# Optimization experiments

Hardware: AMD Instinct MI355X
Metric: run time of the kernel (lower is better)

The kernel has to match this reference:

```python
import jax, jax.numpy as jnp
import numpy as np
from jax import lax

B, T, N, C = 32, 32, 64, 64          # batch, window, num_series, inter_dim
GRU_H, QK, HOR = 64, 32, 12          # gru_dim, qk_dim, prediction_horizon
KS = (3, 5, 7)                       # temporal kernel per block (3 + 2*i)


def setup_inputs() -> dict:
    key = jax.random.key(0)
    ks = jax.random.split(key, 32)
    rn = lambda k, shape, s=0.05: jax.random.normal(k, shape, jnp.float32) * s
    inp = {"x": jax.random.normal(ks[0], (B, T, N), jnp.float32)}
    # x_to_inter_dim: Conv1d(1, C, kernel_size=1) == scalar * w + b
    inp["w_x2i"] = rn(ks[1], (C,)); inp["b_x2i"] = rn(ks[2], (C,))
    # latentCorrelation GRU (input_size=1, hidden=GRU_H), gate order r,z,n
    inp["gru_wih"] = rn(ks[3], (3 * GRU_H, 1)); inp["gru_whh"] = rn(ks[4], (3 * GRU_H, GRU_H))
    inp["gru_bih"] = rn(ks[5], (3 * GRU_H,)); inp["gru_bhh"] = rn(ks[6], (3 * GRU_H,))
    inp["wq_w"] = rn(ks[7], (QK, GRU_H)); inp["wq_b"] = rn(ks[8], (QK,))
    inp["wk_w"] = rn(ks[9], (QK, GRU_H)); inp["wk_b"] = rn(ks[10], (QK,))
    # per block: T independent GCNConvs (theta + bias), one temporal Conv1d
    for i, k_ in enumerate(KS):
        inp[f"gcn_w{i}"] = rn(ks[11 + 4 * i], (T, C, C))
        inp[f"gcn_b{i}"] = rn(ks[12 + 4 * i], (T, C))
        inp[f"conv_w{i}"] = rn(ks[13 + 4 * i], (C, C, k_))
        inp[f"conv_b{i}"] = rn(ks[14 + 4 * i], (C,))
    inp["lout_w"] = rn(ks[25], (N * HOR, T * N * C), 0.01)
    inp["lout_b"] = rn(ks[26], (N * HOR,))
    return inp


def _forward(x, w_x2i, b_x2i, gru_wih, gru_whh, gru_bih, gru_bhh,
             wq_w, wq_b, wk_w, wk_b,
             gcn_w0, gcn_b0, conv_w0, conv_b0,
             gcn_w1, gcn_b1, conv_w1, conv_b1,
             gcn_w2, gcn_b2, conv_w2, conv_b2,
             lout_w, lout_b):
    xs = jnp.transpose(x, (1, 0, 2))  # (T, B, N) time-major

    # --- latentCorrelation: one GRU run over all B*N series at once ---
    def gru_step(h, xt):  # h: (B,N,GRU_H), xt: (B,N)
        gi = xt[..., None] * gru_wih[:, 0] + gru_bih           # (B,N,3H)
        gh = h @ gru_whh.T + gru_bhh                           # (B,N,3H)
        r = jax.nn.sigmoid(gi[..., :GRU_H] + gh[..., :GRU_H])
        z = jax.nn.sigmoid(gi[..., GRU_H:2 * GRU_H] + gh[..., GRU_H:2 * GRU_H])
        n = jnp.tanh(gi[..., 2 * GRU_H:] + r * gh[..., 2 * GRU_H:])
        return (1.0 - z) * n + z * h, None

    h0 = jnp.zeros((B, N, GRU_H), x.dtype)
    hT, _ = lax.scan(gru_step, h0, xs)                         # (B,N,GRU_H)
    Q = hT @ wq_w.T + wq_b                                     # (B,N,QK)
    K = hT @ wk_w.T + wk_b
    Wadj = jax.nn.softmax(jnp.einsum('bnq,bmq->bnm', Q, K) / jnp.sqrt(jnp.float32(QK)), axis=2)

    # GCN symmetric norm on the dense complete graph; edge (src=i, tgt=j) has
    # weight Wadj[b,i,j]; degree is per-target (column) sum.
    deg = Wadj.sum(axis=1)                                     # (B,N)
    dinv = jnp.where(deg > 0, 1.0 / jnp.sqrt(deg), 0.0)
    What = dinv[:, :, None] * Wadj * dinv[:, None, :]          # (B,N,N)

    # x_to_inter_dim (1x1 conv) applied per timestep
    feats = xs[..., None] * w_x2i + b_x2i                      # (T,B,N,C)

    for gw, gb, cw, cb, k_ in ((gcn_w0, gcn_b0, conv_w0, conv_b0, 3),
                               (gcn_w1, gcn_b1, conv_w1, conv_b1, 5),
                               (gcn_w2, gcn_b2, conv_w2, conv_b2, 7)):
        xw = jnp.einsum('tbnc,tcd->tbnd', feats, gw)           # per-timestep theta
        agg = jnp.einsum('bij,tbid->tbjd', What, xw) + gb[:, None, None, :]
        seq = jnp.transpose(agg, (1, 2, 3, 0)).reshape(B * N, C, T)
        p = k_ // 2
        conv = lax.conv_general_dilated(seq, cw, (1,), [(p, p)],
                                        dimension_numbers=('NCH', 'OIH', 'NCH'))
        conv = conv + cb[None, :, None]
        conv = jnp.where(conv >= 0, conv, 0.01 * conv)         # LeakyReLU (dropout p=0)
        feats = jnp.transpose(conv.reshape(B, N, C, T), (3, 0, 1, 2))

    # stack(x_list, dim=2).view(B*N, C*T).view(B, -1) -> (B, N*C*T) feature order (n,c,t)
    flat = jnp.transpose(feats, (1, 2, 3, 0)).reshape(B, N * C * T)
    out = flat @ lout_w.T + lout_b                             # (B, N*HOR)
    return out.reshape(B, HOR, N)


def reference(x, w_x2i, b_x2i, gru_wih, gru_whh, gru_bih, gru_bhh,
              wq_w, wq_b, wk_w, wk_b,
              gcn_w0, gcn_b0, conv_w0, conv_b0,
              gcn_w1, gcn_b1, conv_w1, conv_b1,
              gcn_w2, gcn_b2, conv_w2, conv_b2,
              lout_w, lout_b):
    return _forward(x, w_x2i, b_x2i, gru_wih, gru_whh, gru_bih, gru_bhh,
                    wq_w, wq_b, wk_w, wk_b,
                    gcn_w0, gcn_b0, conv_w0, conv_b0,
                    gcn_w1, gcn_b1, conv_w1, conv_b1,
                    gcn_w2, gcn_b2, conv_w2, conv_b2,
                    lout_w, lout_b)
```

## Files before the change

kernel.cpp:

```cpp
#include <hip/hip_runtime.h>
#include <hip/hip_bf16.h>

#define BB 32
#define TT 32
#define NN 64
#define CC 64
#define HH 64
#define QKD 32
#define HOR 12
#define OUTD (NN*HOR)
#define KFLAT (NN*CC*TT)

typedef __attribute__((ext_vector_type(4))) float f32x4;
typedef __attribute__((ext_vector_type(8))) short s16x8;
typedef unsigned short ush;

static __device__ __forceinline__ ush f2bf(float f) {
    unsigned u = __float_as_uint(f);
    unsigned r = (u + 0x7FFFu + ((u >> 16) & 1u)) >> 16;
    return (ush)r;
}
static __device__ __forceinline__ float bf2f(ush h) {
    return __uint_as_float(((unsigned)h) << 16);
}
static __device__ __forceinline__ void split8(const float* f, uint4& hi, uint4& lo) {
    unsigned hh[8], ll[8];
    #pragma unroll
    for (int i = 0; i < 8; ++i) {
        ush h = f2bf(f[i]);
        float hf = bf2f(h);
        hh[i] = h;
        ll[i] = f2bf(f[i] - hf);
    }
    hi = make_uint4(hh[0] | (hh[1] << 16), hh[2] | (hh[3] << 16),
                    hh[4] | (hh[5] << 16), hh[6] | (hh[7] << 16));
    lo = make_uint4(ll[0] | (ll[1] << 16), ll[2] | (ll[3] << 16),
                    ll[4] | (ll[5] << 16), ll[6] | (ll[7] << 16));
}
static __device__ __forceinline__ void gl2lds16(const void* gsrc, void* ldst) {
    __builtin_amdgcn_global_load_lds(
        (const __attribute__((address_space(1))) unsigned int*)gsrc,
        (__attribute__((address_space(3))) unsigned int*)ldst, 16, 0, 0);
}

__global__ __launch_bounds__(256) void prep_gru_kernel(
    const float* __restrict__ x, const float* __restrict__ wih,
    const float* __restrict__ whh, const float* __restrict__ bih,
    const float* __restrict__ bhh, float* __restrict__ hT,
    const float* __restrict__ gw0, const float* __restrict__ wx, const float* __restrict__ bx,
    float* __restrict__ u, float* __restrict__ v,
    const float* __restrict__ gw1, ush* __restrict__ g1h, ush* __restrict__ g1l,
    const float* __restrict__ gw2, ush* __restrict__ g2h, ush* __restrict__ g2l,
    const float* __restrict__ cw1, ush* __restrict__ c1h, ush* __restrict__ c1l,
    const float* __restrict__ cw2, ush* __restrict__ c2h, ush* __restrict__ c2l,
    const float* __restrict__ cw3, ush* __restrict__ c3h, ush* __restrict__ c3l,
    const float* __restrict__ lb, float* __restrict__ out)
{
    __shared__ __align__(16) char smem[17408];
    int bid = blockIdx.x, tid = threadIdx.x;

    if (bid < 32) {
        float (*pu)[64] = (float(*)[64])smem;
        float (*pv)[64] = (float(*)[64])(smem + 1024);
        int t = bid, d = tid & 63, cq = tid >> 6;
        float su = 0.f, sv = 0.f;
        for (int c = cq*16; c < cq*16 + 16; ++c) {
            float gv = gw0[t*4096 + c*64 + d];
            su += wx[c]*gv; sv += bx[c]*gv;
        }
        pu[cq][d] = su; pv[cq][d] = sv;
        __syncthreads();
        if (tid < 64) {
            u[t*64 + tid] = pu[0][tid]+pu[1][tid]+pu[2][tid]+pu[3][tid];
            v[t*64 + tid] = pv[0][tid]+pv[1][tid]+pv[2][tid]+pv[3][tid];
        }
    } else if (bid < 96) {
        const float* gw = (bid < 64) ? gw1 : gw2;
        ush* hi = (bid < 64) ? g1h : g2h;
        ush* lo = (bid < 64) ? g1l : g2l;
        int t = (bid < 64) ? bid - 32 : bid - 64;
        for (int idx = tid; idx < 4096; idx += 256) {
            int d = idx >> 6, c = idx & 63;
            float val = gw[t*4096 + c*64 + d];
            ush h = f2bf(val);
            hi[t*4096 + idx] = h;
            lo[t*4096 + idx] = f2bf(val - bf2f(h));
        }
    } else if (bid < 288) {
        const float* cw; ush *hi, *lo; int KW, co;
        if (bid < 160)      { cw = cw1; hi = c1h; lo = c1l; KW = 3; co = bid - 96; }
        else if (bid < 224) { cw = cw2; hi = c2h; lo = c2l; KW = 5; co = bid - 160; }
        else                { cw = cw3; hi = c3h; lo = c3l; KW = 7; co = bid - 224; }
        int K = KW*64;
        for (int idx = tid; idx < K; idx += 256) {
            int ka = idx >> 6, ci = idx & 63;
            float val = cw[(size_t)(co*64 + ci)*KW + ka];
            ush h = f2bf(val);
            hi[(size_t)co*K + idx] = h;
            lo[(size_t)co*K + idx] = f2bf(val - bf2f(h));
        }
    } else if (bid < 384) {
        int idx = (bid - 288)*256 + tid;
        out[idx] = lb[idx % OUTD];
    }
    __syncthreads();

    {
        float (*hbuf)[64] = (float(*)[64])smem;
        float4* part = (float4*)(smem + 1024);
        int w = tid >> 6, j = tid & 63;
        float Wreg[3][16];
        #pragma unroll
        for (int g = 0; g < 3; ++g)
            #pragma unroll
            for (int q = 0; q < 4; ++q) {
                float4 wv = *(const float4*)&whh[(g*64 + j)*64 + w*16 + q*4];
                Wreg[g][q*4+0] = wv.x; Wreg[g][q*4+1] = wv.y;
                Wreg[g][q*4+2] = wv.z; Wreg[g][q*4+3] = wv.w;
            }
        hbuf[w][j] = 0.0f;
        int gs0 = bid * 4;
        int b = gs0 >> 6, n0 = gs0 & 63;
        float wih_r = wih[j], wih_z = wih[64+j], wih_n = wih[128+j];
        float bi_r = bih[j], bi_z = bih[64+j], bi_n = bih[128+j];
        float bh_r = bhh[j], bh_z = bhh[64+j], bh_n = bhh[128+j];
        __syncthreads();
        float hreg = 0.0f;
        for (int t = 0; t < TT; ++t) {
            float p[3][4];
            #pragma unroll
            for (int g = 0; g < 3; ++g)
                #pragma unroll
                for (int s = 0; s < 4; ++s) p[g][s] = 0.f;
            #pragma unroll
            for (int s = 0; s < 4; ++s) {
                #pragma unroll
                for (int q = 0; q < 4; ++q) {
                    const float4 hv = *(const float4*)&hbuf[s][w*16 + q*4];
                    #pragma unroll
                    for (int g = 0; g < 3; ++g) {
                        p[g][s] += hv.x*Wreg[g][q*4]   + hv.y*Wreg[g][q*4+1]
                                 + hv.z*Wreg[g][q*4+2] + hv.w*Wreg[g][q*4+3];
                    }
                }
            }
            #pragma unroll
            for (int s = 0; s < 4; ++s)
                part[(w*4 + s)*64 + j] = make_float4(p[0][s], p[1][s], p[2][s], 0.f);
            __syncthreads();
            float4 q0 = part[(0*4 + w)*64 + j];
            float4 q1 = part[(1*4 + w)*64 + j];
            float4 q2 = part[(2*4 + w)*64 + j];
            float4 q3 = part[(3*4 + w)*64 + j];
            float gr = bh_r + q0.x + q1.x + q2.x + q3.x;
            float gz = bh_z + q0.y + q1.y + q2.y + q3.y;
            float gn = bh_n + q0.z + q1.z + q2.z + q3.z;
            float xt = x[(b*TT + t)*NN + n0 + w];
            float r = 1.f/(1.f+__expf(-(xt*wih_r + bi_r + gr)));
            float z = 1.f/(1.f+__expf(-(xt*wih_z + bi_z + gz)));
            float nn_ = tanhf(xt*wih_n + bi_n + r*gn);
            float hnew = (1.f - z)*nn_ + z*hreg;
            hreg = hnew;
            hbuf[w][j] = hnew;
            __syncthreads();
        }
        hT[(gs0 + w)*64 + j] = hreg;
    }
}

__global__ __launch_bounds__(256) void attn_kernel(
    const float* __restrict__ hT, const float* __restrict__ wq_w,
    const float* __restrict__ wq_b, const float* __restrict__ wk_w,
    const float* __restrict__ wk_b,
    ush* __restrict__ whT_hi, ush* __restrict__ whT_lo)
{
    __shared__ float hs[64][64];
    __shared__ float Qs[64][33], Ks[64][33];
    __shared__ float S[64][65];
    __shared__ float pd[4][64];
    __shared__ float dinv[64];
    int b = blockIdx.x, tid = threadIdx.x;
    for (int idx = tid; idx < 64*64; idx += 256) hs[idx>>6][idx&63] = hT[b*4096 + idx];
    __syncthreads();
    for (int idx = tid; idx < 64*32; idx += 256) {
        int n_ = idx >> 5, q = idx & 31;
        float accq = wq_b[q], acck = wk_b[q];
        #pragma unroll 8
        for (int h_ = 0; h_ < 64; ++h_) {
            float hv = hs[n_][h_];
            accq += hv * wq_w[q*64 + h_];
            acck += hv * wk_w[q*64 + h_];
        }
        Qs[n_][q] = accq; Ks[n_][q] = acck;
    }
    __syncthreads();
    const float scale = 0.17677669529663687f;
    for (int idx = tid; idx < 64*64; idx += 256) {
        int n_ = idx >> 6, m = idx & 63;
        float acc = 0.f;
        #pragma unroll 8
        for (int q = 0; q < 32; ++q) acc += Qs[n_][q]*Ks[m][q];
        S[n_][m] = acc * scale;
    }
    __syncthreads();
    {
        int r = tid >> 2, q = tid & 3;
        float mx = -1e30f;
        #pragma unroll
        for (int m = 0; m < 16; ++m) mx = fmaxf(mx, S[r][q*16+m]);
        mx = fmaxf(mx, __shfl_xor(mx, 1));
        mx = fmaxf(mx, __shfl_xor(mx, 2));
        float sum = 0.f;
        float e[16];
        #pragma unroll
        for (int m = 0; m < 16; ++m) { e[m] = __expf(S[r][q*16+m]-mx); sum += e[m]; }
        sum += __shfl_xor(sum, 1);
        sum += __shfl_xor(sum, 2);
        float inv = 1.f/sum;
        #pragma unroll
        for (int m = 0; m < 16; ++m) S[r][q*16+m] = e[m]*inv;
    }
    __syncthreads();
    {
        int c = tid & 63, rq = tid >> 6;
        float d = 0.f;
        #pragma unroll
        for (int i = 0; i < 16; ++i) d += S[rq*16 + i][c];
        pd[rq][c] = d;
    }
    __syncthreads();
    if (tid < 64) {
        float d = pd[0][tid]+pd[1][tid]+pd[2][tid]+pd[3][tid];
        dinv[tid] = (d > 0.f) ? 1.0f/sqrtf(d) : 0.f;
    }
    __syncthreads();
    for (int idx = tid; idx < 64*64; idx += 256) {
        int jj = idx >> 6, ii = idx & 63;
        float val = dinv[ii]*S[ii][jj]*dinv[jj];
        ush h = f2bf(val);
        whT_hi[b*4096 + idx] = h;
        whT_lo[b*4096 + idx] = f2bf(val - bf2f(h));
    }
}

template<bool FIRST>
__global__ __launch_bounds__(256) void gcn_mfma(
    const float* __restrict__ fin,
    const ush* __restrict__ gwT_hi, const ush* __restrict__ gwT_lo,
    const float* __restrict__ u, const float* __restrict__ v,
    const ush* __restrict__ whT_hi, const ush* __restrict__ whT_lo,
    const float* __restrict__ gb, float* __restrict__ o)
{
    __shared__ __align__(16) ush ft_hi[64][64], ft_lo[64][64];
    __shared__ __align__(16) ush xsT_hi[64][64], xsT_lo[64][64];
    __shared__ float x_l[64];
    int tb = blockIdx.x, t = tb >> 5, b = tb & 31;
    int tid = threadIdx.x;
    int w = tid >> 6, l = tid & 63, lm = l & 15, ld = l >> 4;

    if (FIRST) {
        if (tid < 64) x_l[tid] = fin[(b*TT + t)*NN + tid];
        __syncthreads();
        int d = tid >> 2, nq = tid & 3;
        float ud = u[t*64 + d], vd = v[t*64 + d];
        float vals[16];
        #pragma unroll
        for (int i = 0; i < 16; ++i) vals[i] = x_l[nq*16 + i]*ud + vd;
        #pragma unroll
        for (int h = 0; h < 2; ++h) {
            uint4 hi, lo; split8(&vals[h*8], hi, lo);
            int un = (nq*2 + h) ^ (d & 7);
            *(uint4*)&xsT_hi[d][un*8] = hi;
            *(uint4*)&xsT_lo[d][un*8] = lo;
        }
        __syncthreads();
    } else {
        {
            int row = tid >> 2, c0 = (tid & 3) * 16;
            const float* src = fin + (size_t)tb*4096 + row*64 + c0;
            float f8a[8], f8b[8];
            *(float4*)f8a = *(const float4*)src;       *(float4*)(f8a+4) = *(const float4*)(src+4);
            *(float4*)f8b = *(const float4*)(src+8);   *(float4*)(f8b+4) = *(const float4*)(src+12);
            uint4 hi, lo;
            split8(f8a, hi, lo);
            int u0 = ((c0>>3)) ^ (row & 7);
            *(uint4*)&ft_hi[row][u0*8] = hi; *(uint4*)&ft_lo[row][u0*8] = lo;
            split8(f8b, hi, lo);
            int u1 = ((c0>>3)+1) ^ (row & 7);
            *(uint4*)&ft_hi[row][u1*8] = hi; *(uint4*)&ft_lo[row][u1*8] = lo;
        }
        __syncthreads();
        f32x4 acc[4];
        #pragma unroll
        for (int ct = 0; ct < 4; ++ct) acc[ct] = (f32x4){0.f,0.f,0.f,0.f};
        #pragma unroll
        for (int kc = 0; kc < 2; ++kc) {
            int nrow = w*16 + lm;
            int ux = (kc*4 + ld) ^ (nrow & 7);
            s16x8 xh = *(const s16x8*)&ft_hi[nrow][ux*8];
            s16x8 xl = *(const s16x8*)&ft_lo[nrow][ux*8];
            #pragma unroll
            for (int ct = 0; ct < 4; ++ct) {
                int drow = ct*16 + lm;
                s16x8 yh = *(const s16x8*)&gwT_hi[t*4096 + drow*64 + kc*32 + ld*8];
                s16x8 yl = *(const s16x8*)&gwT_lo[t*4096 + drow*64 + kc*32 + ld*8];
                acc[ct] = __builtin_amdgcn_mfma_f32_16x16x32_bf16(xh, yh, acc[ct], 0, 0, 0);
                acc[ct] = __builtin_amdgcn_mfma_f32_16x16x32_bf16(xh, yl, acc[ct], 0, 0, 0);
                acc[ct] = __builtin_amdgcn_mfma_f32_16x16x32_bf16(xl, yh, acc[ct], 0, 0, 0);
            }
        }
        #pragma unroll
        for (int ct = 0; ct < 4; ++ct) {
            int d = ct*16 + lm;
            int n0 = w*16 + ld*4;
            ush hh[4], llo[4];
            #pragma unroll
            for (int r = 0; r < 4; ++r) {
                float val = acc[ct][r];
                ush h = f2bf(val);
                hh[r] = h; llo[r] = f2bf(val - bf2f(h));
            }
            int un = (n0 >> 3) ^ (d & 7);
            int base = d*64 + un*8 + (n0 & 7);
            *(uint2*)&xsT_hi[0][0 + base] = make_uint2(hh[0]|(hh[1]<<16), hh[2]|(hh[3]<<16));
            *(uint2*)&xsT_lo[0][0 + base] = make_uint2(llo[0]|(llo[1]<<16), llo[2]|(llo[3]<<16));
        }
        __syncthreads();
    }

    f32x4 acc2[4];
    #pragma unroll
    for (int ct = 0; ct < 4; ++ct) acc2[ct] = (f32x4){0.f,0.f,0.f,0.f};
    #pragma unroll
    for (int kc = 0; kc < 2; ++kc) {
        int jrow = w*16 + lm;
        s16x8 wh = *(const s16x8*)&whT_hi[b*4096 + jrow*64 + kc*32 + ld*8];
        s16x8 wl = *(const s16x8*)&whT_lo[b*4096 + jrow*64 + kc*32 + ld*8];
        #pragma unroll
        for (int ct = 0; ct < 4; ++ct) {
            int drow = ct*16 + lm;
            int uy = (kc*4 + ld) ^ (drow & 7);
            s16x8 yh = *(const s16x8*)&xsT_hi[drow][uy*8];
            s16x8 yl = *(const s16x8*)&xsT_lo[drow][uy*8];
            acc2[ct] = __builtin_amdgcn_mfma_f32_16x16x32_bf16(wh, yh, acc2[ct], 0, 0, 0);
            acc2[ct] = __builtin_amdgcn_mfma_f32_16x16x32_bf16(wh, yl, acc2[ct], 0, 0, 0);
            acc2[ct] = __builtin_amdgcn_mfma_f32_16x16x32_bf16(wl, yh, acc2[ct], 0, 0, 0);
        }
    }
    float* oo = o + (size_t)tb*4096;
    #pragma unroll
    for (int ct = 0; ct < 4; ++ct) {
        int d = ct*16 + lm;
        float bias = gb[t*64 + d];
        #pragma unroll
        for (int r = 0; r < 4; ++r) {
            int jj = w*16 + ld*4 + r;
            oo[jj*64 + d] = acc2[ct][r] + bias;
        }
    }
}

template<int KW, bool LAST>
__global__ __launch_bounds__(256) void conv_mfma(float* __restrict__ g,
    const ush* __restrict__ wch, const ush* __restrict__ wcl,
    const float* __restrict__ cb, ush* __restrict__ fo)
{
    constexpr int P = KW/2, K = KW*64, K32 = KW*2;
    __shared__ __align__(16) ush sh[32][64], sl[32][64];
    int bn = blockIdx.x, tid = threadIdx.x;
    {
        int t = tid >> 3, c0 = (tid & 7) * 8;
        const float* src = &g[((size_t)t*2048 + bn)*64 + c0];
        float f8[8];
        *(float4*)f8 = *(const float4*)src;
        *(float4*)(f8+4) = *(const float4*)(src+4);
        uint4 hi, lo; split8(f8, hi, lo);
        int uu = (tid & 7) ^ (t & 7);
        *(uint4*)&sh[t][uu*8] = hi;
        *(uint4*)&sl[t][uu*8] = lo;
    }
    __syncthreads();
    int w = tid >> 6, l = tid & 63, lm = l & 15, ld = l >> 4;
    int co = w*16 + lm;
    f32x4 acc0 = {0.f,0.f,0.f,0.f}, acc1 = {0.f,0.f,0.f,0.f};
    const s16x8 zf = {0,0,0,0,0,0,0,0};
    for (int kc = 0; kc < K32; ++kc) {
        int ka = kc >> 1;
        int ci = (kc & 1)*32 + ld*8;
        s16x8 yh = *(const s16x8*)&wch[(size_t)co*K + kc*32 + ld*8];
        s16x8 yl = *(const s16x8*)&wcl[(size_t)co*K + kc*32 + ld*8];
        #pragma unroll
        for (int Mt = 0; Mt < 2; ++Mt) {
            int ts = Mt*16 + lm + ka - P;
            bool ok = ((unsigned)ts) < 32u;
            int tc = ok ? ts : 0;
            int ua = (ci >> 3) ^ (tc & 7);
            s16x8 xh = *(const s16x8*)&sh[tc][ua*8];
            s16x8 xl = *(const s16x8*)&sl[tc][ua*8];
            if (!ok) { xh = zf; xl = zf; }
            f32x4& a = Mt ? acc1 : acc0;
            a = __builtin_amdgcn_mfma_f32_16x16x32_bf16(xh, yh, a, 0, 0, 0);
            a = __builtin_amdgcn_mfma_f32_16x16x32_bf16(xh, yl, a, 0, 0, 0);
            a = __builtin_amdgcn_mfma_f32_16x16x32_bf16(xl, yh, a, 0, 0, 0);
        }
    }
    float bias = cb[co];
    if (LAST) {
        int b = bn >> 6, n = bn & 63;
        ush* ob = fo + (size_t)b*KFLAT + n*2048 + co*32;
        #pragma unroll
        for (int Mt = 0; Mt < 2; ++Mt) {
            const f32x4& a = Mt ? acc1 : acc0;
            ush hv[4];
            #pragma unroll
            for (int r = 0; r < 4; ++r) {
                float val = a[r] + bias;
                val = (val >= 0.f) ? val : 0.01f*val;
                hv[r] = f2bf(val);
            }
            *(uint2*)&ob[Mt*16 + ld*4] = make_uint2(hv[0]|(hv[1]<<16), hv[2]|(hv[3]<<16));
        }
    } else {
        #pragma unroll
        for (int Mt = 0; Mt < 2; ++Mt) {
            const f32x4& a = Mt ? acc1 : acc0;
            #pragma unroll
            for (int r = 0; r < 4; ++r) {
                int t = Mt*16 + ld*4 + r;
                float val = a[r] + bias;
                val = (val >= 0.f) ? val : 0.01f*val;
                g[((size_t)t*2048 + bn)*64 + co] = val;
            }
        }
    }
}

__global__ __launch_bounds__(256) void gemm_mfma(const ush* __restrict__ flat,
                                                 const float* __restrict__ W,
                                                 float* __restrict__ out)
{
    __shared__ __align__(16) float Wl[2][64][64];
    __shared__ __align__(16) ush Al[2][32][64];
    const int tid = threadIdx.x;
    const int w = tid >> 6, l = tid & 63;
    const int og = blockIdx.x >> 6;
    const int kc = blockIdx.x & 63;
    const int o_blk = og * 64;
    const int kbase = kc * 2048;

    const int wrow_l = l >> 4;
    const int wu = l & 15;
    size_t w_off[4];
    #pragma unroll
    for (int i = 0; i < 4; ++i) {
        int row = w*16 + i*4 + wrow_l;
        w_off[i] = (size_t)(o_blk + row) * KFLAT + (unsigned)((wu ^ (row & 7)) * 4);
    }
    const int arow = w*8 + (l >> 3);
    const int au = l & 7;
    const size_t a_off0 = (size_t)arow * KFLAT + (unsigned)((au ^ (arow & 7)) * 8);

#define ISSUE_TILE(buf_, s_) { \
    int kwin_ = kbase + (s_)*64; \
    _Pragma("unroll") \
    for (int i_ = 0; i_ < 4; ++i_) \
        gl2lds16(W + w_off[i_] + kwin_, &Wl[buf_][w*16 + i_*4][0]); \
    gl2lds16(flat + a_off0 + kwin_, &Al[buf_][w*8][0]); \
}

    f32x4 acc0 = {0.f,0.f,0.f,0.f}, acc1 = {0.f,0.f,0.f,0.f};
    ISSUE_TILE(0, 0);
    ISSUE_TILE(1, 1);

    const int lmod = l & 15, ldiv = l >> 4, lx = l & 7;
    for (int s = 0; s < 32; ++s) {
        if (s < 31) { asm volatile("s_waitcnt vmcnt(5)" ::: "memory"); }
        else        { asm volatile("s_waitcnt vmcnt(0)" ::: "memory"); }
        __builtin_amdgcn_s_barrier();
        asm volatile("" ::: "memory");
        const int cur = s & 1;
        #pragma unroll
        for (int ksub = 0; ksub < 2; ++ksub) {
            int ju = ksub*8 + ldiv*2;
            const float4 b0 = *(const float4*)&Wl[cur][w*16 + lmod][(ju ^ lx)*4];
            const float4 b1 = *(const float4*)&Wl[cur][w*16 + lmod][((ju+1) ^ lx)*4];
            float bf[8] = {b0.x,b0.y,b0.z,b0.w,b1.x,b1.y,b1.z,b1.w};
            s16x8 bhi;
            #pragma unroll
            for (int i = 0; i < 8; ++i) bhi[i] = (short)f2bf(bf[i]);
            int jua = ksub*4 + ldiv;
            const s16x8 a0 = *(const s16x8*)&Al[cur][lmod]      [(jua ^ lx)*8];
            const s16x8 a1 = *(const s16x8*)&Al[cur][16 + lmod] [(jua ^ lx)*8];
            acc0 = __builtin_amdgcn_mfma_f32_16x16x32_bf16(a0, bhi, acc0, 0, 0, 0);
            acc1 = __builtin_amdgcn_mfma_f32_16x16x32_bf16(a1, bhi, acc1, 0, 0, 0);
        }
        asm volatile("" ::: "memory");
        __builtin_amdgcn_s_barrier();
        if (s < 30) { ISSUE_TILE(cur, s+2); }
    }
#undef ISSUE_TILE

    const int o_out = o_blk + w*16 + lmod;
    #pragma unroll
    for (int r = 0; r < 4; ++r) {
        int b0_ = ldiv*4 + r;
        atomicAdd(&out[(size_t)b0_*OUTD + o_out], acc0[r]);
        atomicAdd(&out[(size_t)(16 + b0_)*OUTD + o_out], acc1[r]);
    }
}

extern "C" void kernel_launch(void* const* d_in, const int* in_sizes, int n_in,
                              void* d_out, int out_size, void* d_ws, size_t ws_size,
                              hipStream_t stream) {
    (void)in_sizes; (void)n_in; (void)out_size; (void)ws_size;
    const float* x        = (const float*)d_in[0];
    const float* w_x2i    = (const float*)d_in[1];
    const float* b_x2i    = (const float*)d_in[2];
    const float* gru_wih  = (const float*)d_in[3];
    const float* gru_whh  = (const float*)d_in[4];
    const float* gru_bih  = (const float*)d_in[5];
    const float* gru_bhh  = (const float*)d_in[6];
    const float* wq_w     = (const float*)d_in[7];
    const float* wq_b     = (const float*)d_in[8];
    const float* wk_w     = (const float*)d_in[9];
    const float* wk_b     = (const float*)d_in[10];
    const float* gcn_w[3]  = {(const float*)d_in[11], (const float*)d_in[15], (const float*)d_in[19]};
    const float* gcn_b[3]  = {(const float*)d_in[12], (const float*)d_in[16], (const float*)d_in[20]};
    const float* conv_w[3] = {(const float*)d_in[13], (const float*)d_in[17], (const float*)d_in[21]};
    const float* conv_b[3] = {(const float*)d_in[14], (const float*)d_in[18], (const float*)d_in[22]};
    const float* lout_w   = (const float*)d_in[23];
    const float* lout_b   = (const float*)d_in[24];
    float* out = (float*)d_out;
    float* ws  = (float*)d_ws;

    float* hT   = ws;
    float* u    = ws + 131072;
    float* v    = ws + 133120;
    float* bufA = ws + 135168;
    float* bufB = bufA + 4194304;
    ush* usb = (ush*)(ws + 8523776);
    ush* whT_hi  = usb;
    ush* whT_lo  = usb + 131072;
    ush* gwT1_hi = usb + 262144;
    ush* gwT1_lo = usb + 393216;
    ush* gwT2_hi = usb + 524288;
    ush* gwT2_lo = usb + 655360;
    ush* cw1_hi  = usb + 786432;
    ush* cw1_lo  = usb + 798720;
    ush* cw2_hi  = usb + 811008;
    ush* cw2_lo  = usb + 831488;
    ush* cw3_hi  = usb + 851968;
    ush* cw3_lo  = usb + 880640;

    prep_gru_kernel<<<dim3(512), dim3(256), 0, stream>>>(
        x, gru_wih, gru_whh, gru_bih, gru_bhh, hT,
        gcn_w[0], w_x2i, b_x2i, u, v,
        gcn_w[1], gwT1_hi, gwT1_lo,
        gcn_w[2], gwT2_hi, gwT2_lo,
        conv_w[0], cw1_hi, cw1_lo,
        conv_w[1], cw2_hi, cw2_lo,
        conv_w[2], cw3_hi, cw3_lo,
        lout_b, out);
    attn_kernel<<<dim3(32), dim3(256), 0, stream>>>(hT, wq_w, wq_b, wk_w, wk_b, whT_hi, whT_lo);

    unsigned short* flat16 = (unsigned short*)bufB;
    gcn_mfma<true><<<dim3(1024), dim3(256), 0, stream>>>(x, nullptr, nullptr, u, v,
                                                         whT_hi, whT_lo, gcn_b[0], bufA);
    conv_mfma<3,false><<<dim3(2048), dim3(256), 0, stream>>>(bufA, cw1_hi, cw1_lo, conv_b[0], nullptr);
    gcn_mfma<false><<<dim3(1024), dim3(256), 0, stream>>>(bufA, gwT1_hi, gwT1_lo, u, v,
                                                          whT_hi, whT_lo, gcn_b[1], bufB);
    conv_mfma<5,false><<<dim3(2048), dim3(256), 0, stream>>>(bufB, cw2_hi, cw2_lo, conv_b[1], nullptr);
    gcn_mfma<false><<<dim3(1024), dim3(256), 0, stream>>>(bufB, gwT2_hi, gwT2_lo, u, v,
                                                          whT_hi, whT_lo, gcn_b[2], bufA);
    conv_mfma<7,true><<<dim3(2048), dim3(256), 0, stream>>>(bufA, cw3_hi, cw3_lo, conv_b[2], flat16);

    gemm_mfma<<<dim3(768), dim3(256), 0, stream>>>(flat16, lout_w, out);
}
```

Measured before the change: 292.8 us.

## Collapse first GCN+conv block algebraically and register-pipeline final GEMM weights

The first block's input is rank-one per time step (x*u+v), so the GCN and the k=3 temporal conv are folded into precomputed per-(t,co) coefficient tables (Au, Av, Ag) plus a per-batch normalized-adjacency product computed inside the attention kernel. A lightweight fused1_kernel then evaluates the conv output directly. This removes one MFMA GCN launch, one MFMA conv launch and the conv1 weight split. Separately, the final GEMM now loads fp32 weights straight into registers with a 3-deep software pipeline instead of staging them through LDS. This adds register pressure and a serial extra block in the attention kernel.

```diff
diff --git a/kernel.cpp b/kernel.cpp
--- a/kernel.cpp
+++ b/kernel.cpp
@@ -51,7 +51,6 @@
     float* __restrict__ u, float* __restrict__ v,
     const float* __restrict__ gw1, ush* __restrict__ g1h, ush* __restrict__ g1l,
     const float* __restrict__ gw2, ush* __restrict__ g2h, ush* __restrict__ g2l,
-    const float* __restrict__ cw1, ush* __restrict__ c1h, ush* __restrict__ c1l,
     const float* __restrict__ cw2, ush* __restrict__ c2h, ush* __restrict__ c2l,
     const float* __restrict__ cw3, ush* __restrict__ c3h, ush* __restrict__ c3l,
     const float* __restrict__ lb, float* __restrict__ out)
@@ -86,11 +85,10 @@
             hi[t*4096 + idx] = h;
             lo[t*4096 + idx] = f2bf(val - bf2f(h));
         }
-    } else if (bid < 288) {
+    } else if (bid < 224) {
         const float* cw; ush *hi, *lo; int KW, co;
-        if (bid < 160)      { cw = cw1; hi = c1h; lo = c1l; KW = 3; co = bid - 96; }
-        else if (bid < 224) { cw = cw2; hi = c2h; lo = c2l; KW = 5; co = bid - 160; }
-        else                { cw = cw3; hi = c3h; lo = c3l; KW = 7; co = bid - 224; }
+        if (bid < 160) { cw = cw2; hi = c2h; lo = c2l; KW = 5; co = bid - 96; }
+        else           { cw = cw3; hi = c3h; lo = c3l; KW = 7; co = bid - 160; }
         int K = KW*64;
         for (int idx = tid; idx < K; idx += 256) {
             int ka = idx >> 6, ci = idx & 63;
@@ -99,8 +97,8 @@
             hi[(size_t)co*K + idx] = h;
             lo[(size_t)co*K + idx] = f2bf(val - bf2f(h));
         }
-    } else if (bid < 384) {
-        int idx = (bid - 288)*256 + tid;
+    } else if (bid < 320) {
+        int idx = (bid - 224)*256 + tid;
         out[idx] = lb[idx % OUTD];
     }
     __syncthreads();
@@ -172,14 +170,35 @@
     const float* __restrict__ hT, const float* __restrict__ wq_w,
     const float* __restrict__ wq_b, const float* __restrict__ wk_w,
     const float* __restrict__ wk_b,
-    ush* __restrict__ whT_hi, ush* __restrict__ whT_lo)
+    ush* __restrict__ whT_hi, ush* __restrict__ whT_lo,
+    const float* __restrict__ x, float* __restrict__ sbuf, float* __restrict__ dgbuf,
+    const float* __restrict__ u, const float* __restrict__ v,
+    const float* __restrict__ cw1, const float* __restrict__ gb0,
+    float* __restrict__ Au, float* __restrict__ Av, float* __restrict__ Ag)
 {
+    int b = blockIdx.x, tid = threadIdx.x;
+    if (b == 32) {
+        for (int idx = tid; idx < 3*32*64; idx += 256) {
+            int ka = idx >> 11;
+            int t  = (idx >> 6) & 31;
+            int co = idx & 63;
+            float au_ = 0.f, av_ = 0.f, ag_ = 0.f;
+            for (int ci = 0; ci < 64; ++ci) {
+                float w_ = cw1[(size_t)(co*64 + ci)*3 + ka];
+                au_ += w_ * u[t*64 + ci];
+                av_ += w_ * v[t*64 + ci];
+                ag_ += w_ * gb0[t*64 + ci];
+            }
+            Au[idx] = au_; Av[idx] = av_; Ag[idx] = ag_;
+        }
+        return;
+    }
     __shared__ float hs[64][64];
     __shared__ float Qs[64][33], Ks[64][33];
     __shared__ float S[64][65];
     __shared__ float pd[4][64];
     __shared__ float dinv[64];
-    int b = blockIdx.x, tid = threadIdx.x;
+    float (*xl)[64] = (float(*)[64])hs;
     for (int idx = tid; idx < 64*64; idx += 256) hs[idx>>6][idx&63] = hT[b*4096 + idx];
     __syncthreads();
     for (int idx = tid; idx < 64*32; idx += 256) {
@@ -203,6 +222,10 @@
         S[n_][m] = acc * scale;
     }
     __syncthreads();
+    for (int idx = tid; idx < 32*64; idx += 256) {
+        int t = idx >> 6, i = idx & 63;
+        xl[t][i] = x[(b*TT + t)*NN + i];
+    }
     {
         int r = tid >> 2, q = tid & 3;
         float mx = -1e30f;
@@ -235,98 +258,141 @@
     }
     __syncthreads();
     for (int idx = tid; idx < 64*64; idx += 256) {
+        int i = idx >> 6, j = idx & 63;
+        S[i][j] *= dinv[i];
+    }
+    __syncthreads();
+    for (int idx = tid; idx < 64*64; idx += 256) {
         int jj = idx >> 6, ii = idx & 63;
-        float val = dinv[ii]*S[ii][jj]*dinv[jj];
+        float val = S[ii][jj]*dinv[jj];
         ush h = f2bf(val);
         whT_hi[b*4096 + idx] = h;
         whT_lo[b*4096 + idx] = f2bf(val - bf2f(h));
     }
-}
-
-template<bool FIRST>
+    {
+        int c = tid & 63, rq = tid >> 6;
+        float d = 0.f;
+        #pragma unroll
+        for (int i = 0; i < 16; ++i) d += S[rq*16 + i][c];
+        pd[rq][c] = d;
+    }
+    __syncthreads();
+    if (tid < 64) {
+        dgbuf[b*64 + tid] = dinv[tid]*(pd[0][tid]+pd[1][tid]+pd[2][tid]+pd[3][tid]);
+    }
+    {
+        int j = tid & 63, tq = tid >> 6;
+        float acc[8];
+        #pragma unroll
+        for (int uu = 0; uu < 8; ++uu) acc[uu] = 0.f;
+        for (int i = 0; i < 64; ++i) {
+            float rv = S[i][j];
+            #pragma unroll
+            for (int uu = 0; uu < 8; ++uu)
+                acc[uu] += rv * xl[tq*8 + uu][i];
+        }
+        float dj = dinv[j];
+        #pragma unroll
+        for (int uu = 0; uu < 8; ++uu)
+            sbuf[(b*32 + tq*8 + uu)*64 + j] = acc[uu] * dj;
+    }
+}
+
+__global__ __launch_bounds__(256) void fused1_kernel(
+    const float* __restrict__ sbuf, const float* __restrict__ dgbuf,
+    const float* __restrict__ Au, const float* __restrict__ Av, const float* __restrict__ Ag,
+    const float* __restrict__ cb1, float* __restrict__ o)
+{
+    __shared__ float sl[32];
+    __shared__ float dgl;
+    int bn = blockIdx.x, b = bn >> 6, n = bn & 63;
+    int tid = threadIdx.x;
+    if (tid < 32) sl[tid] = sbuf[(b*32 + tid)*64 + n];
+    if (tid == 32) dgl = dgbuf[b*64 + n];
+    __syncthreads();
+    int co = tid & 63, tg = tid >> 6;
+    float cb = cb1[co];
+    float d = dgl;
+    #pragma unroll
+    for (int uu = 0; uu < 8; ++uu) {
+        int t = tg*8 + uu;
+        float acc = cb;
+        #pragma unroll
+        for (int ka = 0; ka < 3; ++ka) {
+            int tp = t + ka - 1;
+            if (tp >= 0 && tp < 32) {
+                int ti = (ka*32 + tp)*64 + co;
+                acc += sl[tp]*Au[ti] + d*Av[ti] + Ag[ti];
+            }
+        }
+        acc = (acc >= 0.f) ? acc : 0.01f*acc;
+        o[((size_t)t*2048 + bn)*64 + co] = acc;
+    }
+}
+
 __global__ __launch_bounds__(256) void gcn_mfma(
     const float* __restrict__ fin,
     const ush* __restrict__ gwT_hi, const ush* __restrict__ gwT_lo,
-    const float* __restrict__ u, const float* __restrict__ v,
     const ush* __restrict__ whT_hi, const ush* __restrict__ whT_lo,
     const float* __restrict__ gb, float* __restrict__ o)
 {
     __shared__ __align__(16) ush ft_hi[64][64], ft_lo[64][64];
     __shared__ __align__(16) ush xsT_hi[64][64], xsT_lo[64][64];
-    __shared__ float x_l[64];
     int tb = blockIdx.x, t = tb >> 5, b = tb & 31;
     int tid = threadIdx.x;
     int w = tid >> 6, l = tid & 63, lm = l & 15, ld = l >> 4;
 
-    if (FIRST) {
-        if (tid < 64) x_l[tid] = fin[(b*TT + t)*NN + tid];
-        __syncthreads();
-        int d = tid >> 2, nq = tid & 3;
-        float ud = u[t*64 + d], vd = v[t*64 + d];
-        float vals[16];
-        #pragma unroll
-        for (int i = 0; i < 16; ++i) vals[i] = x_l[nq*16 + i]*ud + vd;
-        #pragma unroll
-        for (int h = 0; h < 2; ++h) {
-            uint4 hi, lo; split8(&vals[h*8], hi, lo);
-            int un = (nq*2 + h) ^ (d & 7);
-            *(uint4*)&xsT_hi[d][un*8] = hi;
-            *(uint4*)&xsT_lo[d][un*8] = lo;
-        }
-        __syncthreads();
-    } else {
-        {
-            int row = tid >> 2, c0 = (tid & 3) * 16;
-            const float* src = fin + (size_t)tb*4096 + row*64 + c0;
-            float f8a[8], f8b[8];
-            *(float4*)f8a = *(const float4*)src;       *(float4*)(f8a+4) = *(const float4*)(src+4);
-            *(float4*)f8b = *(const float4*)(src+8);   *(float4*)(f8b+4) = *(const float4*)(src+12);
-            uint4 hi, lo;
-            split8(f8a, hi, lo);
-            int u0 = ((c0>>3)) ^ (row & 7);
-            *(uint4*)&ft_hi[row][u0*8] = hi; *(uint4*)&ft_lo[row][u0*8] = lo;
-            split8(f8b, hi, lo);
-            int u1 = ((c0>>3)+1) ^ (row & 7);
-            *(uint4*)&ft_hi[row][u1*8] = hi; *(uint4*)&ft_lo[row][u1*8] = lo;
-        }
-        __syncthreads();
-        f32x4 acc[4];
-        #pragma unroll
-        for (int ct = 0; ct < 4; ++ct) acc[ct] = (f32x4){0.f,0.f,0.f,0.f};
-        #pragma unroll
-        for (int kc = 0; kc < 2; ++kc) {
-            int nrow = w*16 + lm;
-            int ux = (kc*4 + ld) ^ (nrow & 7);
-            s16x8 xh = *(const s16x8*)&ft_hi[nrow][ux*8];
-            s16x8 xl = *(const s16x8*)&ft_lo[nrow][ux*8];
-            #pragma unroll
-            for (int ct = 0; ct < 4; ++ct) {
-                int drow = ct*16 + lm;
-                s16x8 yh = *(const s16x8*)&gwT_hi[t*4096 + drow*64 + kc*32 + ld*8];
-                s16x8 yl = *(const s16x8*)&gwT_lo[t*4096 + drow*64 + kc*32 + ld*8];
-                acc[ct] = __builtin_amdgcn_mfma_f32_16x16x32_bf16(xh, yh, acc[ct], 0, 0, 0);
-                acc[ct] = __builtin_amdgcn_mfma_f32_16x16x32_bf16(xh, yl, acc[ct], 0, 0, 0);
-                acc[ct] = __builtin_amdgcn_mfma_f32_16x16x32_bf16(xl, yh, acc[ct], 0, 0, 0);
-            }
-        }
+    {
+        int row = tid >> 2, c0 = (tid & 3) * 16;
+        const float* src = fin + (size_t)tb*4096 + row*64 + c0;
+        float f8a[8], f8b[8];
+        *(float4*)f8a = *(const float4*)src;       *(float4*)(f8a+4) = *(const float4*)(src+4);
+        *(float4*)f8b = *(const float4*)(src+8);   *(float4*)(f8b+4) = *(const float4*)(src+12);
+        uint4 hi, lo;
+        split8(f8a, hi, lo);
+        int u0 = ((c0>>3)) ^ (row & 7);
+        *(uint4*)&ft_hi[row][u0*8] = hi; *(uint4*)&ft_lo[row][u0*8] = lo;
+        split8(f8b, hi, lo);
+        int u1 = ((c0>>3)+1) ^ (row & 7);
+        *(uint4*)&ft_hi[row][u1*8] = hi; *(uint4*)&ft_lo[row][u1*8] = lo;
+    }
+    __syncthreads();
+    f32x4 acc[4];
+    #pragma unroll
+    for (int ct = 0; ct < 4; ++ct) acc[ct] = (f32x4){0.f,0.f,0.f,0.f};
+    #pragma unroll
+    for (int kc = 0; kc < 2; ++kc) {
+        int nrow = w*16 + lm;
+        int ux = (kc*4 + ld) ^ (nrow & 7);
+        s16x8 xh = *(const s16x8*)&ft_hi[nrow][ux*8];
+        s16x8 xl = *(const s16x8*)&ft_lo[nrow][ux*8];
         #pragma unroll
         for (int ct = 0; ct < 4; ++ct) {
-            int d = ct*16 + lm;
-            int n0 = w*16 + ld*4;
-            ush hh[4], llo[4];
-            #pragma unroll
-            for (int r = 0; r < 4; ++r) {
-                float val = acc[ct][r];
-                ush h = f2bf(val);
-                hh[r] = h; llo[r] = f2bf(val - bf2f(h));
-            }
-            int un = (n0 >> 3) ^ (d & 7);
-            int base = d*64 + un*8 + (n0 & 7);
-            *(uint2*)&xsT_hi[0][0 + base] = make_uint2(hh[0]|(hh[1]<<16), hh[2]|(hh[3]<<16));
-            *(uint2*)&xsT_lo[0][0 + base] = make_uint2(llo[0]|(llo[1]<<16), llo[2]|(llo[3]<<16));
-        }
-        __syncthreads();
-    }
+            int drow = ct*16 + lm;
+            s16x8 yh = *(const s16x8*)&gwT_hi[t*4096 + drow*64 + kc*32 + ld*8];
+            s16x8 yl = *(const s16x8*)&gwT_lo[t*4096 + drow*64 + kc*32 + ld*8];
+            acc[ct] = __builtin_amdgcn_mfma_f32_16x16x32_bf16(xh, yh, acc[ct], 0, 0, 0);
+            acc[ct] = __builtin_amdgcn_mfma_f32_16x16x32_bf16(xh, yl, acc[ct], 0, 0, 0);
+            acc[ct] = __builtin_amdgcn_mfma_f32_16x16x32_bf16(xl, yh, acc[ct], 0, 0, 0);
+        }
+    }
+    #pragma unroll
+    for (int ct = 0; ct < 4; ++ct) {
+        int d = ct*16 + lm;
+        int n0 = w*16 + ld*4;
+        ush hh[4], llo[4];
+        #pragma unroll
+        for (int r = 0; r < 4; ++r) {
+            float val = acc[ct][r];
+            ush h = f2bf(val);
+            hh[r] = h; llo[r] = f2bf(val - bf2f(h));
+        }
+        int un = (n0 >> 3) ^ (d & 7);
+        int base = d*64 + un*8 + (n0 & 7);
+        *(uint2*)&xsT_hi[0][0 + base] = make_uint2(hh[0]|(hh[1]<<16), hh[2]|(hh[3]<<16));
+        *(uint2*)&xsT_lo[0][0 + base] = make_uint2(llo[0]|(llo[1]<<16), llo[2]|(llo[3]<<16));
+    }
+    __syncthreads();
 
     f32x4 acc2[4];
     #pragma unroll
@@ -439,66 +505,73 @@
                                                  const float* __restrict__ W,
                                                  float* __restrict__ out)
 {
-    __shared__ __align__(16) float Wl[2][64][64];
-    __shared__ __align__(16) ush Al[2][32][64];
+    __shared__ __align__(16) ush Al[4][32][64];
     const int tid = threadIdx.x;
     const int w = tid >> 6, l = tid & 63;
     const int og = blockIdx.x >> 6;
     const int kc = blockIdx.x & 63;
     const int o_blk = og * 64;
     const int kbase = kc * 2048;
-
-    const int wrow_l = l >> 4;
-    const int wu = l & 15;
-    size_t w_off[4];
-    #pragma unroll
-    for (int i = 0; i < 4; ++i) {
-        int row = w*16 + i*4 + wrow_l;
-        w_off[i] = (size_t)(o_blk + row) * KFLAT + (unsigned)((wu ^ (row & 7)) * 4);
-    }
+    const int lmod = l & 15, ldiv = l >> 4, lx = l & 7;
+
     const int arow = w*8 + (l >> 3);
     const int au = l & 7;
-    const size_t a_off0 = (size_t)arow * KFLAT + (unsigned)((au ^ (arow & 7)) * 8);
-
-#define ISSUE_TILE(buf_, s_) { \
-    int kwin_ = kbase + (s_)*64; \
+    const ush* aptr = flat + (size_t)arow*KFLAT + (unsigned)((au ^ (arow & 7))*8) + kbase;
+    const float* wptr = W + (size_t)(o_blk + w*16 + lmod)*KFLAT + kbase + ldiv*8;
+
+    float4 wr0[4], wr1[4], wr2[4];
+#define LOADW(dst_, s_) { \
+    dst_[0] = *(const float4*)(wptr + (s_)*64);      \
+    dst_[1] = *(const float4*)(wptr + (s_)*64 + 4);  \
+    dst_[2] = *(const float4*)(wptr + (s_)*64 + 32); \
+    dst_[3] = *(const float4*)(wptr + (s_)*64 + 36); }
+#define ISSUEA(s_) gl2lds16(aptr + (s_)*64, &Al[(s_)&3][w*8][0]);
+
+    f32x4 acc0 = {0.f,0.f,0.f,0.f}, acc1 = {0.f,0.f,0.f,0.f};
+
+#define COMPUTE(wr_, s_) { \
+    const int abuf_ = (s_) & 3; \
     _Pragma("unroll") \
-    for (int i_ = 0; i_ < 4; ++i_) \
-        gl2lds16(W + w_off[i_] + kwin_, &Wl[buf_][w*16 + i_*4][0]); \
-    gl2lds16(flat + a_off0 + kwin_, &Al[buf_][w*8][0]); \
-}
-
-    f32x4 acc0 = {0.f,0.f,0.f,0.f}, acc1 = {0.f,0.f,0.f,0.f};
-    ISSUE_TILE(0, 0);
-    ISSUE_TILE(1, 1);
-
-    const int lmod = l & 15, ldiv = l >> 4, lx = l & 7;
-    for (int s = 0; s < 32; ++s) {
-        if (s < 31) { asm volatile("s_waitcnt vmcnt(5)" ::: "memory"); }
-        else        { asm volatile("s_waitcnt vmcnt(0)" ::: "memory"); }
+    for (int ksub = 0; ksub < 2; ++ksub) { \
+        float bf_[8] = {wr_[ksub*2].x, wr_[ksub*2].y, wr_[ksub*2].z, wr_[ksub*2].w, \
+                        wr_[ksub*2+1].x, wr_[ksub*2+1].y, wr_[ksub*2+1].z, wr_[ksub*2+1].w}; \
+        s16x8 bhi_; \
+        _Pragma("unroll") \
+        for (int i_ = 0; i_ < 8; ++i_) bhi_[i_] = (short)f2bf(bf_[i_]); \
+        int jua_ = ksub*4 + ldiv; \
+        const s16x8 a0_ = *(const s16x8*)&Al[abuf_][lmod]     [(jua_ ^ lx)*8]; \
+        const s16x8 a1_ = *(const s16x8*)&Al[abuf_][16 + lmod][(jua_ ^ lx)*8]; \
+        acc0 = __builtin_amdgcn_mfma_f32_16x16x32_bf16(a0_, bhi_, acc0, 0, 0, 0); \
+        acc1 = __builtin_amdgcn_mfma_f32_16x16x32_bf16(a1_, bhi_, acc1, 0, 0, 0); \
+    } }
+
+    LOADW(wr0, 0); ISSUEA(0);
+    LOADW(wr1, 1); ISSUEA(1);
+    LOADW(wr2, 2); ISSUEA(2);
+
+    for (int s = 0; s < 30; s += 3) {
+        asm volatile("s_waitcnt vmcnt(10)" ::: "memory");
         __builtin_amdgcn_s_barrier();
-        asm volatile("" ::: "memory");
-        const int cur = s & 1;
-        #pragma unroll
-        for (int ksub = 0; ksub < 2; ++ksub) {
-            int ju = ksub*8 + ldiv*2;
-            const float4 b0 = *(const float4*)&Wl[cur][w*16 + lmod][(ju ^ lx)*4];
-            const float4 b1 = *(const float4*)&Wl[cur][w*16 + lmod][((ju+1) ^ lx)*4];
-            float bf[8] = {b0.x,b0.y,b0.z,b0.w,b1.x,b1.y,b1.z,b1.w};
-            s16x8 bhi;
-            #pragma unroll
-            for (int i = 0; i < 8; ++i) bhi[i] = (short)f2bf(bf[i]);
-            int jua = ksub*4 + ldiv;
-            const s16x8 a0 = *(const s16x8*)&Al[cur][lmod]      [(jua ^ lx)*8];
-            const s16x8 a1 = *(const s16x8*)&Al[cur][16 + lmod] [(jua ^ lx)*8];
-            acc0 = __builtin_amdgcn_mfma_f32_16x16x32_bf16(a0, bhi, acc0, 0, 0, 0);
-            acc1 = __builtin_amdgcn_mfma_f32_16x16x32_bf16(a1, bhi, acc1, 0, 0, 0);
-        }
-        asm volatile("" ::: "memory");
+        COMPUTE(wr0, s);
+        if (s + 3 < 32) { LOADW(wr0, s+3); ISSUEA(s+3); }
+        asm volatile("s_waitcnt vmcnt(10)" ::: "memory");
         __builtin_amdgcn_s_barrier();
-        if (s < 30) { ISSUE_TILE(cur, s+2); }
-    }
-#undef ISSUE_TILE
+        COMPUTE(wr1, s+1);
+        if (s + 4 < 32) { LOADW(wr1, s+4); ISSUEA(s+4); }
+        asm volatile("s_waitcnt vmcnt(10)" ::: "memory");
+        __builtin_amdgcn_s_barrier();
+        COMPUTE(wr2, s+2);
+        if (s + 5 < 32) { LOADW(wr2, s+5); ISSUEA(s+5); }
+    }
+    asm volatile("s_waitcnt vmcnt(5)" ::: "memory");
+    __builtin_amdgcn_s_barrier();
+    COMPUTE(wr0, 30);
+    asm volatile("s_waitcnt vmcnt(0)" ::: "memory");
+    __builtin_amdgcn_s_barrier();
+    COMPUTE(wr1, 31);
+#undef LOADW
+#undef ISSUEA
+#undef COMPUTE
 
     const int o_out = o_blk + w*16 + lmod;
     #pragma unroll
@@ -545,33 +618,37 @@
     ush* gwT1_lo = usb + 393216;
     ush* gwT2_hi = usb + 524288;
     ush* gwT2_lo = usb + 655360;
-    ush* cw1_hi  = usb + 786432;
-    ush* cw1_lo  = usb + 798720;
-    ush* cw2_hi  = usb + 811008;
-    ush* cw2_lo  = usb + 831488;
-    ush* cw3_hi  = usb + 851968;
-    ush* cw3_lo  = usb + 880640;
+    ush* cw2_hi  = usb + 786432;
+    ush* cw2_lo  = usb + 806912;
+    ush* cw3_hi  = usb + 827392;
+    ush* cw3_lo  = usb + 856064;
+    float* fxtra = ws + 8523776 + 442368;
+    float* sbuf  = fxtra;
+    float* dgbuf = fxtra + 65536;
+    float* Au    = fxtra + 67584;
+    float* Av    = fxtra + 73728;
+    float* Ag    = fxtra + 79872;
 
     prep_gru_kernel<<<dim3(512), dim3(256), 0, stream>>>(
         x, gru_wih, gru_whh, gru_bih, gru_bhh, hT,
         gcn_w[0], w_x2i, b_x2i, u, v,
         gcn_w[1], gwT1_hi, gwT1_lo,
         gcn_w[2], gwT2_hi, gwT2_lo,
-        conv_w[0], cw1_hi, cw1_lo,
         conv_w[1], cw2_hi, cw2_lo,
         conv_w[2], cw3_hi, cw3_lo,
         lout_b, out);
-    attn_kernel<<<dim3(32), dim3(256), 0, stream>>>(hT, wq_w, wq_b, wk_w, wk_b, whT_hi, whT_lo);
+    attn_kernel<<<dim3(33), dim3(256), 0, stream>>>(
+        hT, wq_w, wq_b, wk_w, wk_b, whT_hi, whT_lo,
+        x, sbuf, dgbuf, u, v, conv_w[0], gcn_b[0], Au, Av, Ag);
 
     unsigned short* flat16 = (unsigned short*)bufB;
-    gcn_mfma<true><<<dim3(1024), dim3(256), 0, stream>>>(x, nullptr, nullptr, u, v,
-                                                         whT_hi, whT_lo, gcn_b[0], bufA);
-    conv_mfma<3,false><<<dim3(2048), dim3(256), 0, stream>>>(bufA, cw1_hi, cw1_lo, conv_b[0], nullptr);
-    gcn_mfma<false><<<dim3(1024), dim3(256), 0, stream>>>(bufA, gwT1_hi, gwT1_lo, u, v,
-                                                          whT_hi, whT_lo, gcn_b[1], bufB);
+    fused1_kernel<<<dim3(2048), dim3(256), 0, stream>>>(sbuf, dgbuf, Au, Av, Ag,
+                                                        conv_b[0], bufA);
+    gcn_mfma<<<dim3(1024), dim3(256), 0, stream>>>(bufA, gwT1_hi, gwT1_lo,
+                                                   whT_hi, whT_lo, gcn_b[1], bufB);
     conv_mfma<5,false><<<dim3(2048), dim3(256), 0, stream>>>(bufB, cw2_hi, cw2_lo, conv_b[1], nullptr);
-    gcn_mfma<false><<<dim3(1024), dim3(256), 0, stream>>>(bufB, gwT2_hi, gwT2_lo, u, v,
-                                                          whT_hi, whT_lo, gcn_b[2], bufA);
+    gcn_mfma<<<dim3(1024), dim3(256), 0, stream>>>(bufB, gwT2_hi, gwT2_lo,
+                                                   whT_hi, whT_lo, gcn_b[2], bufA);
     conv_mfma<7,true><<<dim3(2048), dim3(256), 0, stream>>>(bufA, cw3_hi, cw3_lo, conv_b[2], flat16);
 
     gemm_mfma<<<dim3(768), dim3(256), 0, stream>>>(flat16, lout_w, out);
```

Result: slower. 441.5 us (+50.8%).
